# Performance work log

Measured on AMD Instinct MI355X. Metric: run time of the kernel, lower is better.

Reference implementation:

```python
import jax, jax.numpy as jnp
import numpy as np

TAU = 2.0          # LIF membrane time constant (spikingjelly default)
ALPHA = 2.0        # ATan surrogate width
EPS = 1e-5         # BatchNorm eps
NUM_HEADS = 8
SCALE = 0.125

@jax.custom_vjp
def spike(x):
    return (x >= 0.0).astype(x.dtype)

def _spike_fwd(x):
    return (x >= 0.0).astype(x.dtype), x

def _spike_bwd(x, g):
    # ATan surrogate gradient (spikingjelly default)
    return (g * (ALPHA / 2.0) / (1.0 + (jnp.pi / 2.0 * ALPHA * x) ** 2),)

spike.defvjp(_spike_fwd, _spike_bwd)

def lif(x, v_th):
    # Multi-step LIF over leading time axis T; hard reset to 0, v_reset=0.
    def step(v, xt):
        h = v + (xt - v) / TAU
        s = spike(h - v_th)
        return h * (1.0 - s), s
    _, s = jax.lax.scan(step, jnp.zeros_like(x[0]), x)
    return s

def bn(x, g, b, m, v):
    # BatchNorm1d in eval mode over channel (last) dim
    return (x - m) * jax.lax.rsqrt(v + EPS) * g + b

def setup_inputs() -> dict:
    key = jax.random.key(0)
    ks = jax.random.split(key, 16)
    T, B, N, C = 4, 16, 512, 512
    s = 1.0 / np.sqrt(C)
    inp = {"x": jax.random.normal(ks[0], (T, B, N, C), jnp.float32)}
    for i, p in enumerate("qkvp"):
        inp[f"w{p}"] = jax.random.normal(ks[1 + i], (C, C), jnp.float32) * s
        inp[f"b{p}"] = jnp.zeros((C,), jnp.float32)
        inp[f"{p}_gamma"] = jnp.ones((C,), jnp.float32)
        inp[f"{p}_beta"] = jnp.zeros((C,), jnp.float32)
        inp[f"{p}_mean"] = jax.random.normal(ks[5 + i], (C,), jnp.float32) * 0.1
        inp[f"{p}_var"] = jax.random.uniform(ks[9 + i], (C,), jnp.float32, minval=0.5, maxval=1.5)
    return inp

def reference(x, wq, bq, q_gamma, q_beta, q_mean, q_var,
              wk, bk, k_gamma, k_beta, k_mean, k_var,
              wv, bv, v_gamma, v_beta, v_mean, v_var,
              wp, bp, p_gamma, p_beta, p_mean, p_var):
    T, B, N, C = x.shape
    H = NUM_HEADS
    D = C // H

    def branch(w, b, g, be, m, va):
        y = bn(x @ w.T + b, g, be, m, va)          # Linear -> BN1d (eval)
        y = lif(y, 1.0)                             # spiking activation
        return y.reshape(T, B, N, H, D).transpose(0, 1, 3, 2, 4)  # [T,B,H,N,D]

    q = branch(wq, bq, q_gamma, q_beta, q_mean, q_var)
    k = branch(wk, bk, k_gamma, k_beta, k_mean, k_var)
    v = branch(wv, bv, v_gamma, v_beta, v_mean, v_var)

    attn = jnp.einsum('tbhnd,tbhmd->tbhnm', q, k) * SCALE  # [T,B,H,N,N]
    o = jnp.einsum('tbhnm,tbhmd->tbhnd', attn, v)          # [T,B,H,N,D]
    o = o.transpose(0, 1, 3, 2, 4).reshape(T, B, N, C)
    o = lif(o, 0.5)                                        # attn_lif, v_th=0.5
    o = bn(o @ wp.T + bp, p_gamma, p_beta, p_mean, p_var)
    return lif(o, 1.0)
```

## Files before the change

kernel.cpp:

```cpp
#include <hip/hip_runtime.h>
#include <hip/hip_bf16.h>
#include <hip/hip_fp16.h>
#include <cstddef>
#include <cstdint>

#define T_ 4
#define B_ 16
#define N_ 512
#define C_ 512
#define H_ 8
#define D_ 64
#define BN_T (B_*N_)

typedef unsigned short u16;
typedef __attribute__((ext_vector_type(8))) short bf16x8;
typedef __attribute__((ext_vector_type(8))) _Float16 f16x8;
typedef __attribute__((ext_vector_type(8))) unsigned short u16x8;
typedef __attribute__((ext_vector_type(4))) float f32x4;

__device__ __forceinline__ u16 f2bf_exact(float f) {
    union { float f; unsigned u; } x; x.f = f; return (u16)(x.u >> 16);
}
__device__ __forceinline__ void split2(float f, u16& h1, u16& h2) {
    const __half a = __float2half(f);
    const float r = (f - __half2float(a)) * 2048.0f;
    const __half b = __float2half(r);
    h1 = __half_as_ushort(a); h2 = __half_as_ushort(b);
}
__device__ __forceinline__ int swz(int rr, int q) {
    return (rr << 6) + (((q ^ ((rr >> 1) & 3)) & 3) << 4);
}
__device__ __forceinline__ int SW(int row, int col) {
    return (row << 6) + (col ^ ((row & 7) << 3));
}
__device__ __forceinline__ void gload16(const void* g, void* l) {
    __builtin_amdgcn_global_load_lds(
        (const __attribute__((address_space(1))) unsigned int*)g,
        (__attribute__((address_space(3))) unsigned int*)l, 16, 0, 0);
}

#define PHASE2T(p, STAGE, WAIT) do {                                          \
    const int cc_ = 64 * wc + 16 * (p);                                       \
    const int rrB_ = (cc_ & 127) + l15;                                       \
    const char* LB_ = L + (1 + (cc_ >> 7)) * 8192;                            \
    const f16x8 b1_ = *reinterpret_cast<const f16x8*>(LB_ + swz(rrB_, g));    \
    const f16x8 b2_ = *reinterpret_cast<const f16x8*>(LB_ + 16384 + swz(rrB_, g)); \
    STAGE;                                                                    \
    WAIT;                                                                     \
    __builtin_amdgcn_sched_barrier(0);                                        \
    __builtin_amdgcn_s_barrier();                                             \
    asm volatile("s_waitcnt lgkmcnt(0)" ::: "memory");                        \
    __builtin_amdgcn_sched_barrier(0);                                        \
    __builtin_amdgcn_s_setprio(1);                                            \
    _Pragma("unroll")                                                         \
    for (int rt_ = 0; rt_ < 4; ++rt_) {                                       \
        accA[rt_][p] = __builtin_amdgcn_mfma_f32_16x16x32_f16(a1[rt_], b1_, accA[rt_][p], 0, 0, 0); \
        accB[rt_][p] = __builtin_amdgcn_mfma_f32_16x16x32_f16(a1[rt_], b2_, accB[rt_][p], 0, 0, 0); \
    }                                                                         \
    __builtin_amdgcn_s_setprio(0);                                            \
    __builtin_amdgcn_s_barrier();                                             \
} while (0)

__global__ __launch_bounds__(256) void k_split_all(
    const float* __restrict__ x,
    const float* __restrict__ w0, const float* __restrict__ w1,
    const float* __restrict__ w2, const float* __restrict__ w3,
    u16* __restrict__ x1t, u16* __restrict__ x2t, u16* __restrict__ wt)
{
    const int tid = threadIdx.x;
    const int rr = tid >> 1, kh = tid & 1;
    const size_t WSZ = (size_t)C_ * C_;

    const float* src;
    char *d1, *d2;
    if (blockIdx.x < 4096) {
        const int tile = blockIdx.x;
        const int mt = tile >> 4, kb = tile & 15;
        const int t = rr & 3, bn = mt * 32 + (rr >> 2);
        src = x + ((size_t)t * BN_T + bn) * C_ + kb * 32 + kh * 16;
        d1 = (char*)(x1t + ((size_t)tile << 12));
        d2 = (char*)(x2t + ((size_t)tile << 12));
    } else {
        const int r = blockIdx.x - 4096;
        const int wi = r >> 6;
        const int tile = r & 63;
        const int nt = tile >> 4, kb = tile & 15;
        const int c = nt * 128 + rr;
        const float* w = wi == 0 ? w0 : wi == 1 ? w1 : wi == 2 ? w2 : w3;
        src = w + (size_t)c * C_ + kb * 32 + kh * 16;
        d1 = (char*)(wt + (size_t)(2 * wi) * WSZ + ((size_t)tile << 12));
        d2 = (char*)(wt + (size_t)(2 * wi + 1) * WSZ + ((size_t)tile << 12));
    }

    float f[16];
    *reinterpret_cast<float4*>(f + 0)  = *reinterpret_cast<const float4*>(src + 0);
    *reinterpret_cast<float4*>(f + 4)  = *reinterpret_cast<const float4*>(src + 4);
    *reinterpret_cast<float4*>(f + 8)  = *reinterpret_cast<const float4*>(src + 8);
    *reinterpret_cast<float4*>(f + 12) = *reinterpret_cast<const float4*>(src + 12);
    #pragma unroll
    for (int j = 0; j < 2; ++j) {
        u16x8 p1, p2;
        #pragma unroll
        for (int e = 0; e < 8; ++e) { u16 h1, h2; split2(f[8*j+e], h1, h2); p1[e] = h1; p2[e] = h2; }
        const int q = 2 * kh + j;
        *reinterpret_cast<u16x8*>(d1 + swz(rr, q)) = p1;
        *reinterpret_cast<u16x8*>(d2 + swz(rr, q)) = p2;
    }
}

__global__ __launch_bounds__(256, 2) void k_linear_qkv(
    const u16* __restrict__ a1t, const u16* __restrict__ a2t,
    const u16* __restrict__ wt_base,
    const float* __restrict__ bi0, const float* __restrict__ ga0, const float* __restrict__ be0,
    const float* __restrict__ mu0, const float* __restrict__ va0,
    const float* __restrict__ bi1, const float* __restrict__ ga1, const float* __restrict__ be1,
    const float* __restrict__ mu1, const float* __restrict__ va1,
    const float* __restrict__ bi2, const float* __restrict__ ga2, const float* __restrict__ be2,
    const float* __restrict__ mu2, const float* __restrict__ va2,
    u16* __restrict__ oq, u16* __restrict__ ok, u16* __restrict__ ov)
{
    __shared__ u16 lds[2][4][4096];

    const int dd  = blockIdx.x;
    const int lid = (dd & 7) * 384 + (dd >> 3);
    const int mt  = lid / 12;
    const int ntg = lid - mt * 12;
    const int li  = ntg >> 2;
    const int nt  = ntg & 3;
    const int bn0 = mt * 32;
    const int c0  = nt * 128;

    const float* bias  = li == 0 ? bi0 : li == 1 ? bi1 : bi2;
    const float* gamma = li == 0 ? ga0 : li == 1 ? ga1 : ga2;
    const float* beta  = li == 0 ? be0 : li == 1 ? be1 : be2;
    const float* mean  = li == 0 ? mu0 : li == 1 ? mu1 : mu2;
    const float* var   = li == 0 ? va0 : li == 1 ? va1 : va2;
    u16* outp = li == 0 ? oq : li == 1 ? ok : ov;

    const size_t WSZ = (size_t)C_ * C_;
    const u16* w1t = wt_base + (size_t)(2 * li) * WSZ;
    const u16* w2t = wt_base + (size_t)(2 * li + 1) * WSZ;

    const int tid = threadIdx.x;
    const int wv  = tid >> 6, lane = tid & 63;
    const int l15 = lane & 15, g = (lane >> 4) & 3;
    const int wr  = wv >> 1, wc = wv & 1;
    const int go  = wv * 2048 + lane * 16;
    const int lo  = wv * 2048;

    f32x4 accA[4][4], accB[4][4];
    #pragma unroll
    for (int rt = 0; rt < 4; ++rt)
        #pragma unroll
        for (int ct = 0; ct < 4; ++ct) { accA[rt][ct] = {0,0,0,0}; accB[rt][ct] = {0,0,0,0}; }

    const size_t abase = (size_t)mt * 16, bbase = (size_t)nt * 16;

    auto stage = [&](int buf, int kb) {
        char* L = (char*)&lds[buf][0][0];
        const char* ga1p = (const char*)(a1t + ((abase + kb) << 12)) + go;
        const char* ga2p = (const char*)(a2t + ((abase + kb) << 12)) + go;
        const char* gb1 = (const char*)(w1t + ((bbase + kb) << 12)) + go;
        const char* gb2 = (const char*)(w2t + ((bbase + kb) << 12)) + go;
        gload16(ga1p,        L + lo);
        gload16(ga1p + 1024, L + lo + 1024);
        gload16(ga2p,        L + 8192 + lo);
        gload16(ga2p + 1024, L + 8192 + lo + 1024);
        gload16(gb1,        L + 16384 + lo);
        gload16(gb1 + 1024, L + 16384 + lo + 1024);
        gload16(gb2,        L + 24576 + lo);
        gload16(gb2 + 1024, L + 24576 + lo + 1024);
    };

    stage(0, 0);
    __syncthreads();

    #pragma unroll 1
    for (int kb = 0; kb < 16; ++kb) {
        const int buf = kb & 1;
        if (kb < 15) stage(buf ^ 1, kb + 1);
        const char* L = (const char*)&lds[buf][0][0];
        f16x8 a1[4], a2[4];
        #pragma unroll
        for (int rt = 0; rt < 4; ++rt) {
            const int rr = 64 * wr + 16 * rt + l15;
            a1[rt] = *reinterpret_cast<const f16x8*>(L + swz(rr, g));
            a2[rt] = *reinterpret_cast<const f16x8*>(L + 8192 + swz(rr, g));
        }
        #pragma unroll
        for (int ct = 0; ct < 4; ++ct) {
            const int rr2 = 64 * wc + 16 * ct + l15;
            const f16x8 b1 = *reinterpret_cast<const f16x8*>(L + 16384 + swz(rr2, g));
            const f16x8 b2 = *reinterpret_cast<const f16x8*>(L + 24576 + swz(rr2, g));
            #pragma unroll
            for (int rt = 0; rt < 4; ++rt) {
                accA[rt][ct] = __builtin_amdgcn_mfma_f32_16x16x32_f16(a1[rt], b1, accA[rt][ct], 0, 0, 0);
                accB[rt][ct] = __builtin_amdgcn_mfma_f32_16x16x32_f16(a2[rt], b1, accB[rt][ct], 0, 0, 0);
                accB[rt][ct] = __builtin_amdgcn_mfma_f32_16x16x32_f16(a1[rt], b2, accB[rt][ct], 0, 0, 0);
            }
        }
        __syncthreads();
    }

    #pragma unroll
    for (int ct = 0; ct < 4; ++ct) {
        const int c = c0 + 64 * wc + 16 * ct + l15;
        const float rs = 1.0f / sqrtf(var[c] + 1e-5f);
        const float ga = gamma[c], be = beta[c], mu = mean[c], bi = bias[c];
        #pragma unroll
        for (int rt = 0; rt < 4; ++rt) {
            const int bn = bn0 + 16 * wr + 4 * rt + g;
            float vm = 0.f;
            #pragma unroll
            for (int r = 0; r < 4; ++r) {
                const float y = accA[rt][ct][r] + accB[rt][ct][r] * (1.0f / 2048.0f) + bi;
                const float ybn = (y - mu) * rs * ga + be;
                const float h = vm + (ybn - vm) * 0.5f;
                const bool sp = (h >= 1.0f);
                vm = sp ? 0.f : h;
                const int b = bn >> 9, n = bn & 511;
                const int hh = c >> 6, d2 = c & 63;
                outp[((((size_t)r * B_ + b) * H_ + hh) * N_ + n) * D_ + d2] = sp ? 0x3F80 : 0;
            }
        }
    }
}

__global__ __launch_bounds__(512, 2) void k_linear_out(
    const u16* __restrict__ a1t,
    const u16* __restrict__ w1t, const u16* __restrict__ w2t,
    const float* __restrict__ bias, const float* __restrict__ gamma,
    const float* __restrict__ beta, const float* __restrict__ mean,
    const float* __restrict__ var, float* __restrict__ outp)
{
    __shared__ u16 lds[3][5][4096];

    const int dd  = blockIdx.x;
    const int lid = (dd & 7) * 64 + (dd >> 3);
    const int mt  = lid >> 1;
    const int nt  = lid & 1;
    const int bn0 = mt * 32;
    const int c0  = nt * 256;

    const int tid = threadIdx.x;
    const int wv  = tid >> 6, lane = tid & 63;
    const int l15 = lane & 15, g = (lane >> 4) & 3;
    const int wr  = wv >> 2, wc = wv & 3;
    const int so  = tid * 16;

    f32x4 accA[4][4], accB[4][4];
    #pragma unroll
    for (int rt = 0; rt < 4; ++rt)
        #pragma unroll
        for (int ct = 0; ct < 4; ++ct) { accA[rt][ct] = {0,0,0,0}; accB[rt][ct] = {0,0,0,0}; }

    const size_t abase  = (size_t)mt * 16;
    const size_t bbase0 = (size_t)(nt * 2 + 0) * 16;
    const size_t bbase1 = (size_t)(nt * 2 + 1) * 16;
    char* const L0 = (char*)&lds[0][0][0];

    auto s0 = [&](int kb) { char* Ls = L0 + (kb % 3) * 40960;
        gload16((const char*)(a1t + ((abase  + kb) << 12)) + so, Ls + 0 * 8192 + so);
        gload16((const char*)(w1t + ((bbase0 + kb) << 12)) + so, Ls + 1 * 8192 + so); };
    auto s1 = [&](int kb) { char* Ls = L0 + (kb % 3) * 40960;
        gload16((const char*)(w1t + ((bbase1 + kb) << 12)) + so, Ls + 2 * 8192 + so);
        gload16((const char*)(w2t + ((bbase0 + kb) << 12)) + so, Ls + 3 * 8192 + so); };
    auto s2 = [&](int kb) { char* Ls = L0 + (kb % 3) * 40960;
        gload16((const char*)(w2t + ((bbase1 + kb) << 12)) + so, Ls + 4 * 8192 + so); };

    s0(0); s1(0); s2(0);
    s0(1); s1(1); s2(1);
    __builtin_amdgcn_sched_barrier(0);
    asm volatile("s_waitcnt vmcnt(5)" ::: "memory");
    __builtin_amdgcn_s_barrier();
    __builtin_amdgcn_sched_barrier(0);

    #pragma unroll 1
    for (int k = 0; k < 16; ++k) {
        const char* L = L0 + (k % 3) * 40960;
        f16x8 a1[4];
        #pragma unroll
        for (int rt = 0; rt < 4; ++rt) {
            const int rr = 64 * wr + 16 * rt + l15;
            a1[rt] = *reinterpret_cast<const f16x8*>(L + swz(rr, g));
        }
        const bool st = (k <= 13);
        PHASE2T(0, if (st) s0(k + 2), );
        PHASE2T(1, if (st) s1(k + 2), );
        PHASE2T(2, if (st) s2(k + 2), );
        if (k < 14) { PHASE2T(3, , asm volatile("s_waitcnt vmcnt(5)" ::: "memory")); }
        else        { PHASE2T(3, , asm volatile("s_waitcnt vmcnt(0)" ::: "memory")); }
    }

    #pragma unroll
    for (int ct = 0; ct < 4; ++ct) {
        const int c = c0 + 64 * wc + 16 * ct + l15;
        const float rs = 1.0f / sqrtf(var[c] + 1e-5f);
        const float ga = gamma[c], be = beta[c], mu = mean[c], bi = bias[c];
        #pragma unroll
        for (int rt = 0; rt < 4; ++rt) {
            const int bn = bn0 + 16 * wr + 4 * rt + g;
            float vm = 0.f;
            #pragma unroll
            for (int r = 0; r < 4; ++r) {
                const float y = accA[rt][ct][r] + accB[rt][ct][r] * (1.0f / 2048.0f) + bi;
                const float ybn = (y - mu) * rs * ga + be;
                const float h = vm + (ybn - vm) * 0.5f;
                const bool sp = (h >= 1.0f);
                vm = sp ? 0.f : h;
                outp[((size_t)r * BN_T + bn) * C_ + c] = sp ? 1.0f : 0.0f;
            }
        }
    }
}

__global__ __launch_bounds__(512, 2) void k_attn_mfma(
    const u16* __restrict__ qg, const u16* __restrict__ kg,
    const u16* __restrict__ vg, u16* __restrict__ s2t)
{
    __shared__ u16 kf[8][4096];
    __shared__ u16 vf[8][4096];
    __shared__ u16 ssb[8][1024];

    const int id  = blockIdx.x;
    const int lid = (id & 7) * 64 + (id >> 3);
    const int bh  = lid >> 2;
    const int qt  = lid & 3;
    const int b   = bh >> 3, hh = bh & 7;

    const int tid  = threadIdx.x;
    const int w    = tid >> 6, lane = tid & 63;
    const int l15  = lane & 15, g = lane >> 4;

    const int vkv = (tid & 15) * 4;
    const int vd  = ((tid >> 4) & 15) * 4;

    bf16x8 qa[2];
    f32x4 vmem[4], oacc[4];
    #pragma unroll
    for (int d0 = 0; d0 < 4; ++d0) { vmem[d0] = {0,0,0,0}; oacc[d0] = {0,0,0,0}; }

    #pragma unroll 1
    for (int t = 0; t < T_; ++t) {
        const size_t base = ((size_t)t * (B_ * H_) + bh) * (size_t)(N_ * D_);
        if (t > 0) __syncthreads();

        {
            const size_t qrow = base + (size_t)(qt * 128 + 16 * w + l15) * D_;
            qa[0] = *reinterpret_cast<const bf16x8*>(qg + qrow + 8 * g);
            qa[1] = *reinterpret_cast<const bf16x8*>(qg + qrow + 32 + 8 * g);
        }
        {
            const u16* kb = kg + base;
            #pragma unroll
            for (int i = 0; i < 8; ++i) {
                const int r64 = tid >> 3;
                const int col = (tid & 7) * 8;
                const u16x8 v = *reinterpret_cast<const u16x8*>(kb + ((size_t)(tid + 512 * i)) * 8);
                *reinterpret_cast<u16x8*>(&kf[i][SW(r64, col)]) = v;
            }
        }
        {
            const u16* vb = vg + base;
            #pragma unroll
            for (int i = 0; i < 4; ++i) {
                const int jt = 2 * i + (tid >> 8);
                const int m0 = jt * 64;
                ushort4 r0 = *reinterpret_cast<const ushort4*>(vb + (size_t)(m0 + vkv + 0) * D_ + vd);
                ushort4 r1 = *reinterpret_cast<const ushort4*>(vb + (size_t)(m0 + vkv + 1) * D_ + vd);
                ushort4 r2 = *reinterpret_cast<const ushort4*>(vb + (size_t)(m0 + vkv + 2) * D_ + vd);
                ushort4 r3 = *reinterpret_cast<const ushort4*>(vb + (size_t)(m0 + vkv + 3) * D_ + vd);
                ushort4 wv4;
                wv4.x = r0.x; wv4.y = r1.x; wv4.z = r2.x; wv4.w = r3.x;
                *reinterpret_cast<ushort4*>(&vf[jt][SW(vd + 0, vkv)]) = wv4;
                wv4.x = r0.y; wv4.y = r1.y; wv4.z = r2.y; wv4.w = r3.y;
                *reinterpret_cast<ushort4*>(&vf[jt][SW(vd + 1, vkv)]) = wv4;
                wv4.x = r0.z; wv4.y = r1.z; wv4.z = r2.z; wv4.w = r3.z;
                *reinterpret_cast<ushort4*>(&vf[jt][SW(vd + 2, vkv)]) = wv4;
                wv4.x = r0.w; wv4.y = r1.w; wv4.z = r2.w; wv4.w = r3.w;
                *reinterpret_cast<ushort4*>(&vf[jt][SW(vd + 3, vkv)]) = wv4;
            }
        }
        __syncthreads();

        u16* sb = &ssb[w][0];
        #pragma unroll
        for (int jt = 0; jt < 8; ++jt) {
            __builtin_amdgcn_s_setprio(1);
            #pragma unroll
            for (int kvt = 0; kvt < 2; ++kvt) {
                f32x4 acc = {0.f, 0.f, 0.f, 0.f};
                #pragma unroll
                for (int c = 0; c < 2; ++c) {
                    const bf16x8 kb = *reinterpret_cast<const bf16x8*>(
                        &kf[jt][SW(16 * kvt + l15, 32 * c + 8 * g)]);
                    acc = __builtin_amdgcn_mfma_f32_16x16x32_bf16(qa[c], kb, acc, 0, 0, 0);
                }
                #pragma unroll
                for (int r = 0; r < 4; ++r)
                    sb[SW(4 * g + r, 16 * kvt + l15)] = f2bf_exact(acc[r]);
            }
            {
                const bf16x8 sa = *reinterpret_cast<const bf16x8*>(&sb[SW(l15, 8 * g)]);
                #pragma unroll
                for (int d0 = 0; d0 < 4; ++d0) {
                    const bf16x8 vb2 = *reinterpret_cast<const bf16x8*>(
                        &vf[jt][SW(16 * d0 + l15, 8 * g)]);
                    oacc[d0] = __builtin_amdgcn_mfma_f32_16x16x32_bf16(sa, vb2, oacc[d0], 0, 0, 0);
                }
            }
            #pragma unroll
            for (int kvt = 2; kvt < 4; ++kvt) {
                f32x4 acc = {0.f, 0.f, 0.f, 0.f};
                #pragma unroll
                for (int c = 0; c < 2; ++c) {
                    const bf16x8 kb = *reinterpret_cast<const bf16x8*>(
                        &kf[jt][SW(16 * kvt + l15, 32 * c + 8 * g)]);
                    acc = __builtin_amdgcn_mfma_f32_16x16x32_bf16(qa[c], kb, acc, 0, 0, 0);
                }
                #pragma unroll
                for (int r = 0; r < 4; ++r)
                    sb[SW(4 * g + r, 16 * kvt + l15)] = f2bf_exact(acc[r]);
            }
            {
                const bf16x8 sa = *reinterpret_cast<const bf16x8*>(&sb[SW(l15, 32 + 8 * g)]);
                #pragma unroll
                for (int d0 = 0; d0 < 4; ++d0) {
                    const bf16x8 vb2 = *reinterpret_cast<const bf16x8*>(
                        &vf[jt][SW(16 * d0 + l15, 32 + 8 * g)]);
                    oacc[d0] = __builtin_amdgcn_mfma_f32_16x16x32_bf16(sa, vb2, oacc[d0], 0, 0, 0);
                }
            }
            __builtin_amdgcn_s_setprio(0);
        }

        #pragma unroll
        for (int d0 = 0; d0 < 4; ++d0) {
            const int c = hh * 64 + d0 * 16 + l15;
            const int kb2 = c >> 5, kq = (c >> 3) & 3, e = c & 7;
            #pragma unroll
            for (int r = 0; r < 4; ++r) {
                const float o = oacc[d0][r] * 0.125f;
                const float h = vmem[d0][r] + (o - vmem[d0][r]) * 0.5f;
                const bool sp = (h >= 0.5f);
                vmem[d0][r] = sp ? 0.f : h;
                const int n = qt * 128 + 16 * w + 4 * g + r;
                const int bn = b * 512 + n;
                const int mt2 = bn >> 5;
                const int rr2 = (bn & 31) * 4 + t;
                const size_t off = (((size_t)mt2 * 16 + kb2) << 13) + (rr2 << 6)
                                 + (((kq ^ ((rr2 >> 1) & 3)) & 3) << 4) + (e << 1);
                *(u16*)((char*)s2t + off) = sp ? 0x3C00 : 0;
            }
            oacc[d0] = {0.f, 0.f, 0.f, 0.f};
        }
    }
}

extern "C" void kernel_launch(void* const* d_in, const int* in_sizes, int n_in,
                              void* d_out, int out_size, void* d_ws, size_t ws_size,
                              hipStream_t stream)
{
    const float* x = (const float*)d_in[0];
    const float* W[4]  = {(const float*)d_in[1],  (const float*)d_in[7],  (const float*)d_in[13], (const float*)d_in[19]};
    const float* Bi[4] = {(const float*)d_in[2],  (const float*)d_in[8],  (const float*)d_in[14], (const float*)d_in[20]};
    const float* Ga[4] = {(const float*)d_in[3],  (const float*)d_in[9],  (const float*)d_in[15], (const float*)d_in[21]};
    const float* Be[4] = {(const float*)d_in[4],  (const float*)d_in[10], (const float*)d_in[16], (const float*)d_in[22]};
    const float* Mu[4] = {(const float*)d_in[5],  (const float*)d_in[11], (const float*)d_in[17], (const float*)d_in[23]};
    const float* Va[4] = {(const float*)d_in[6],  (const float*)d_in[12], (const float*)d_in[18], (const float*)d_in[24]};

    const size_t SPK = (size_t)T_ * B_ * N_ * C_;
    const size_t WSZ = (size_t)C_ * C_;
    u16* qb  = (u16*)d_ws;
    u16* kbf = qb + SPK;
    u16* vbf = kbf + SPK;
    u16* x1t = vbf + SPK;
    u16* x2t = x1t + SPK;
    u16* wt  = x2t + SPK;
    u16* s2t = x1t;

    dim3 blk(256);
    k_split_all<<<4352, blk, 0, stream>>>(x, W[0], W[1], W[2], W[3], x1t, x2t, wt);

    k_linear_qkv<<<3072, blk, 0, stream>>>(x1t, x2t, wt,
        Bi[0], Ga[0], Be[0], Mu[0], Va[0],
        Bi[1], Ga[1], Be[1], Mu[1], Va[1],
        Bi[2], Ga[2], Be[2], Mu[2], Va[2],
        qb, kbf, vbf);
    k_attn_mfma<<<512, dim3(512), 0, stream>>>(qb, kbf, vbf, s2t);
    k_linear_out<<<512, dim3(512), 0, stream>>>(s2t, wt + 6*WSZ, wt + 7*WSZ,
        Bi[3], Ga[3], Be[3], Mu[3], Va[3], (float*)d_out);
}
```

Measured before the change: 297.6 us.

## Retile output linear to 256-thread blocks and prefetch next timestep in attention

The output projection kernel is retiled from 512-thread blocks covering 256 output columns with a triple-buffered, phase-interleaved pipeline to 256-thread blocks covering 128 columns with a simple double-buffered loop and twice as many blocks. Separately, the attention kernel now issues global loads of K, V and Q for timestep t+1 into registers while timestep t computes, hiding global latency. The register prefetch raises VGPR pressure in the attention kernel and may reduce occupancy. The simpler output GEMM pipeline drops the fine-grained barrier scheduling of the old version.

```diff
diff --git a/kernel.cpp b/kernel.cpp
--- a/kernel.cpp
+++ b/kernel.cpp
@@ -38,28 +38,6 @@
         (const __attribute__((address_space(1))) unsigned int*)g,
         (__attribute__((address_space(3))) unsigned int*)l, 16, 0, 0);
 }
-
-#define PHASE2T(p, STAGE, WAIT) do {                                          \
-    const int cc_ = 64 * wc + 16 * (p);                                       \
-    const int rrB_ = (cc_ & 127) + l15;                                       \
-    const char* LB_ = L + (1 + (cc_ >> 7)) * 8192;                            \
-    const f16x8 b1_ = *reinterpret_cast<const f16x8*>(LB_ + swz(rrB_, g));    \
-    const f16x8 b2_ = *reinterpret_cast<const f16x8*>(LB_ + 16384 + swz(rrB_, g)); \
-    STAGE;                                                                    \
-    WAIT;                                                                     \
-    __builtin_amdgcn_sched_barrier(0);                                        \
-    __builtin_amdgcn_s_barrier();                                             \
-    asm volatile("s_waitcnt lgkmcnt(0)" ::: "memory");                        \
-    __builtin_amdgcn_sched_barrier(0);                                        \
-    __builtin_amdgcn_s_setprio(1);                                            \
-    _Pragma("unroll")                                                         \
-    for (int rt_ = 0; rt_ < 4; ++rt_) {                                       \
-        accA[rt_][p] = __builtin_amdgcn_mfma_f32_16x16x32_f16(a1[rt_], b1_, accA[rt_][p], 0, 0, 0); \
-        accB[rt_][p] = __builtin_amdgcn_mfma_f32_16x16x32_f16(a1[rt_], b2_, accB[rt_][p], 0, 0, 0); \
-    }                                                                         \
-    __builtin_amdgcn_s_setprio(0);                                            \
-    __builtin_amdgcn_s_barrier();                                             \
-} while (0)
 
 __global__ __launch_bounds__(256) void k_split_all(
     const float* __restrict__ x,
@@ -226,27 +204,28 @@
     }
 }
 
-__global__ __launch_bounds__(512, 2) void k_linear_out(
+__global__ __launch_bounds__(256, 2) void k_linear_out(
     const u16* __restrict__ a1t,
     const u16* __restrict__ w1t, const u16* __restrict__ w2t,
     const float* __restrict__ bias, const float* __restrict__ gamma,
     const float* __restrict__ beta, const float* __restrict__ mean,
     const float* __restrict__ var, float* __restrict__ outp)
 {
-    __shared__ u16 lds[3][5][4096];
+    __shared__ u16 lds[2][3][4096];
 
     const int dd  = blockIdx.x;
-    const int lid = (dd & 7) * 64 + (dd >> 3);
-    const int mt  = lid >> 1;
-    const int nt  = lid & 1;
+    const int lid = (dd & 7) * 128 + (dd >> 3);
+    const int mt  = lid >> 2;
+    const int nt  = lid & 3;
     const int bn0 = mt * 32;
-    const int c0  = nt * 256;
+    const int c0  = nt * 128;
 
     const int tid = threadIdx.x;
     const int wv  = tid >> 6, lane = tid & 63;
     const int l15 = lane & 15, g = (lane >> 4) & 3;
-    const int wr  = wv >> 2, wc = wv & 3;
-    const int so  = tid * 16;
+    const int wr  = wv >> 1, wc = wv & 1;
+    const int go  = wv * 2048 + lane * 16;
+    const int lo  = wv * 2048;
 
     f32x4 accA[4][4], accB[4][4];
     #pragma unroll
@@ -254,42 +233,47 @@
         #pragma unroll
         for (int ct = 0; ct < 4; ++ct) { accA[rt][ct] = {0,0,0,0}; accB[rt][ct] = {0,0,0,0}; }
 
-    const size_t abase  = (size_t)mt * 16;
-    const size_t bbase0 = (size_t)(nt * 2 + 0) * 16;
-    const size_t bbase1 = (size_t)(nt * 2 + 1) * 16;
-    char* const L0 = (char*)&lds[0][0][0];
-
-    auto s0 = [&](int kb) { char* Ls = L0 + (kb % 3) * 40960;
-        gload16((const char*)(a1t + ((abase  + kb) << 12)) + so, Ls + 0 * 8192 + so);
-        gload16((const char*)(w1t + ((bbase0 + kb) << 12)) + so, Ls + 1 * 8192 + so); };
-    auto s1 = [&](int kb) { char* Ls = L0 + (kb % 3) * 40960;
-        gload16((const char*)(w1t + ((bbase1 + kb) << 12)) + so, Ls + 2 * 8192 + so);
-        gload16((const char*)(w2t + ((bbase0 + kb) << 12)) + so, Ls + 3 * 8192 + so); };
-    auto s2 = [&](int kb) { char* Ls = L0 + (kb % 3) * 40960;
-        gload16((const char*)(w2t + ((bbase1 + kb) << 12)) + so, Ls + 4 * 8192 + so); };
-
-    s0(0); s1(0); s2(0);
-    s0(1); s1(1); s2(1);
-    __builtin_amdgcn_sched_barrier(0);
-    asm volatile("s_waitcnt vmcnt(5)" ::: "memory");
-    __builtin_amdgcn_s_barrier();
-    __builtin_amdgcn_sched_barrier(0);
+    const size_t abase = (size_t)mt * 16, bbase = (size_t)nt * 16;
+
+    auto stage = [&](int buf, int kb) {
+        char* L = (char*)&lds[buf][0][0];
+        const char* ga1 = (const char*)(a1t + ((abase + kb) << 12)) + go;
+        const char* gb1 = (const char*)(w1t + ((bbase + kb) << 12)) + go;
+        const char* gb2 = (const char*)(w2t + ((bbase + kb) << 12)) + go;
+        gload16(ga1,        L + lo);
+        gload16(ga1 + 1024, L + lo + 1024);
+        gload16(gb1,        L + 8192 + lo);
+        gload16(gb1 + 1024, L + 8192 + lo + 1024);
+        gload16(gb2,        L + 16384 + lo);
+        gload16(gb2 + 1024, L + 16384 + lo + 1024);
+    };
+
+    stage(0, 0);
+    __syncthreads();
 
     #pragma unroll 1
-    for (int k = 0; k < 16; ++k) {
-        const char* L = L0 + (k % 3) * 40960;
+    for (int kb = 0; kb < 16; ++kb) {
+        const int buf = kb & 1;
+        if (kb < 15) stage(buf ^ 1, kb + 1);
+        const char* L = (const char*)&lds[buf][0][0];
         f16x8 a1[4];
         #pragma unroll
         for (int rt = 0; rt < 4; ++rt) {
             const int rr = 64 * wr + 16 * rt + l15;
             a1[rt] = *reinterpret_cast<const f16x8*>(L + swz(rr, g));
         }
-        const bool st = (k <= 13);
-        PHASE2T(0, if (st) s0(k + 2), );
-        PHASE2T(1, if (st) s1(k + 2), );
-        PHASE2T(2, if (st) s2(k + 2), );
-        if (k < 14) { PHASE2T(3, , asm volatile("s_waitcnt vmcnt(5)" ::: "memory")); }
-        else        { PHASE2T(3, , asm volatile("s_waitcnt vmcnt(0)" ::: "memory")); }
+        #pragma unroll
+        for (int ct = 0; ct < 4; ++ct) {
+            const int rr2 = 64 * wc + 16 * ct + l15;
+            const f16x8 b1 = *reinterpret_cast<const f16x8*>(L + 8192 + swz(rr2, g));
+            const f16x8 b2 = *reinterpret_cast<const f16x8*>(L + 16384 + swz(rr2, g));
+            #pragma unroll
+            for (int rt = 0; rt < 4; ++rt) {
+                accA[rt][ct] = __builtin_amdgcn_mfma_f32_16x16x32_f16(a1[rt], b1, accA[rt][ct], 0, 0, 0);
+                accB[rt][ct] = __builtin_amdgcn_mfma_f32_16x16x32_f16(a1[rt], b2, accB[rt][ct], 0, 0, 0);
+            }
+        }
+        __syncthreads();
     }
 
     #pragma unroll
@@ -335,53 +319,62 @@
     const int vkv = (tid & 15) * 4;
     const int vd  = ((tid >> 4) & 15) * 4;
 
-    bf16x8 qa[2];
+    u16x8  kpre[8];
+    ushort4 vpre[4][4];
+    bf16x8 qpre[2], qa[2];
     f32x4 vmem[4], oacc[4];
     #pragma unroll
     for (int d0 = 0; d0 < 4; ++d0) { vmem[d0] = {0,0,0,0}; oacc[d0] = {0,0,0,0}; }
+
+    auto prefetch = [&](int t2) {
+        const size_t base2 = ((size_t)t2 * (B_ * H_) + bh) * (size_t)(N_ * D_);
+        const u16* kb = kg + base2;
+        #pragma unroll
+        for (int i = 0; i < 8; ++i)
+            kpre[i] = *reinterpret_cast<const u16x8*>(kb + ((size_t)(tid + 512 * i)) * 8);
+        const u16* vb = vg + base2;
+        #pragma unroll
+        for (int i = 0; i < 4; ++i) {
+            const int jt = 2 * i + (tid >> 8);
+            const int m0 = jt * 64;
+            #pragma unroll
+            for (int r = 0; r < 4; ++r)
+                vpre[i][r] = *reinterpret_cast<const ushort4*>(vb + (size_t)(m0 + vkv + r) * D_ + vd);
+        }
+        const size_t qrow = base2 + (size_t)(qt * 128 + 16 * w + l15) * D_;
+        qpre[0] = *reinterpret_cast<const bf16x8*>(qg + qrow + 8 * g);
+        qpre[1] = *reinterpret_cast<const bf16x8*>(qg + qrow + 32 + 8 * g);
+    };
+
+    prefetch(0);
 
     #pragma unroll 1
     for (int t = 0; t < T_; ++t) {
-        const size_t base = ((size_t)t * (B_ * H_) + bh) * (size_t)(N_ * D_);
         if (t > 0) __syncthreads();
-
-        {
-            const size_t qrow = base + (size_t)(qt * 128 + 16 * w + l15) * D_;
-            qa[0] = *reinterpret_cast<const bf16x8*>(qg + qrow + 8 * g);
-            qa[1] = *reinterpret_cast<const bf16x8*>(qg + qrow + 32 + 8 * g);
-        }
-        {
-            const u16* kb = kg + base;
-            #pragma unroll
-            for (int i = 0; i < 8; ++i) {
-                const int r64 = tid >> 3;
-                const int col = (tid & 7) * 8;
-                const u16x8 v = *reinterpret_cast<const u16x8*>(kb + ((size_t)(tid + 512 * i)) * 8);
-                *reinterpret_cast<u16x8*>(&kf[i][SW(r64, col)]) = v;
-            }
-        }
-        {
-            const u16* vb = vg + base;
-            #pragma unroll
-            for (int i = 0; i < 4; ++i) {
-                const int jt = 2 * i + (tid >> 8);
-                const int m0 = jt * 64;
-                ushort4 r0 = *reinterpret_cast<const ushort4*>(vb + (size_t)(m0 + vkv + 0) * D_ + vd);
-                ushort4 r1 = *reinterpret_cast<const ushort4*>(vb + (size_t)(m0 + vkv + 1) * D_ + vd);
-                ushort4 r2 = *reinterpret_cast<const ushort4*>(vb + (size_t)(m0 + vkv + 2) * D_ + vd);
-                ushort4 r3 = *reinterpret_cast<const ushort4*>(vb + (size_t)(m0 + vkv + 3) * D_ + vd);
-                ushort4 wv4;
-                wv4.x = r0.x; wv4.y = r1.x; wv4.z = r2.x; wv4.w = r3.x;
-                *reinterpret_cast<ushort4*>(&vf[jt][SW(vd + 0, vkv)]) = wv4;
-                wv4.x = r0.y; wv4.y = r1.y; wv4.z = r2.y; wv4.w = r3.y;
-                *reinterpret_cast<ushort4*>(&vf[jt][SW(vd + 1, vkv)]) = wv4;
-                wv4.x = r0.z; wv4.y = r1.z; wv4.z = r2.z; wv4.w = r3.z;
-                *reinterpret_cast<ushort4*>(&vf[jt][SW(vd + 2, vkv)]) = wv4;
-                wv4.x = r0.w; wv4.y = r1.w; wv4.z = r2.w; wv4.w = r3.w;
-                *reinterpret_cast<ushort4*>(&vf[jt][SW(vd + 3, vkv)]) = wv4;
-            }
+        qa[0] = qpre[0]; qa[1] = qpre[1];
+
+        #pragma unroll
+        for (int i = 0; i < 8; ++i) {
+            const int r64 = tid >> 3;
+            const int col = (tid & 7) * 8;
+            *reinterpret_cast<u16x8*>(&kf[i][SW(r64, col)]) = kpre[i];
+        }
+        #pragma unroll
+        for (int i = 0; i < 4; ++i) {
+            const int jt = 2 * i + (tid >> 8);
+            ushort4 wv4;
+            wv4.x = vpre[i][0].x; wv4.y = vpre[i][1].x; wv4.z = vpre[i][2].x; wv4.w = vpre[i][3].x;
+            *reinterpret_cast<ushort4*>(&vf[jt][SW(vd + 0, vkv)]) = wv4;
+            wv4.x = vpre[i][0].y; wv4.y = vpre[i][1].y; wv4.z = vpre[i][2].y; wv4.w = vpre[i][3].y;
+            *reinterpret_cast<ushort4*>(&vf[jt][SW(vd + 1, vkv)]) = wv4;
+            wv4.x = vpre[i][0].z; wv4.y = vpre[i][1].z; wv4.z = vpre[i][2].z; wv4.w = vpre[i][3].z;
+            *reinterpret_cast<ushort4*>(&vf[jt][SW(vd + 2, vkv)]) = wv4;
+            wv4.x = vpre[i][0].w; wv4.y = vpre[i][1].w; wv4.z = vpre[i][2].w; wv4.w = vpre[i][3].w;
+            *reinterpret_cast<ushort4*>(&vf[jt][SW(vd + 3, vkv)]) = wv4;
         }
         __syncthreads();
+
+        if (t < 3) prefetch(t + 1);
 
         u16* sb = &ssb[w][0];
         #pragma unroll
@@ -488,6 +481,6 @@
         Bi[2], Ga[2], Be[2], Mu[2], Va[2],
         qb, kbf, vbf);
     k_attn_mfma<<<512, dim3(512), 0, stream>>>(qb, kbf, vbf, s2t);
-    k_linear_out<<<512, dim3(512), 0, stream>>>(s2t, wt + 6*WSZ, wt + 7*WSZ,
+    k_linear_out<<<1024, blk, 0, stream>>>(s2t, wt + 6*WSZ, wt + 7*WSZ,
         Bi[3], Ga[3], Be[3], Mu[3], Va[3], (float*)d_out);
 }
```

Result: faster. 276.1 us (-7.2%).
